# Performance work log

Measured on AMD Instinct MI355X. Metric: run time of the kernel, lower is better.

## Reference

```python
import jax, jax.numpy as jnp
import numpy as np

N = 207      # node_size (METR-LA)
E = 1722     # edge_size from edge CSV
RES = 12     # resolution
T = 288 // RES  # time-of-day slots


def setup_inputs() -> dict:
    key = jax.random.key(0)
    ks = jax.random.split(key, 12)
    B, L = 64, 2048
    return {
        "inputs": jax.random.normal(ks[0], (B, 2, N, L), jnp.float32),
        "ind": jax.random.randint(ks[1], (B,), 0, 288),
        "edge_from": jax.random.randint(ks[2], (E,), 0, N),
        "edge_to": jax.random.randint(ks[3], (E,), 0, N),
        "weight_react": jax.random.normal(ks[4], (T, E), jnp.float32) / 10.0,
        "weight_diff": jax.random.normal(ks[5], (T, E), jnp.float32) / 1000.0,
        "weight_react_a": jax.random.normal(ks[6], (T, E), jnp.float32) / 10.0,
        "weight_diff_a": jax.random.normal(ks[7], (T, E), jnp.float32) / 1000.0,
        "bias_reaction": jax.random.normal(ks[8], (T, N), jnp.float32) / 10.0,
        "bias_diffusion": jax.random.normal(ks[9], (T, N), jnp.float32) / 10.0,
        "bias_reaction_a": jax.random.normal(ks[10], (T, N), jnp.float32) / 10.0,
        "bias_diffusion_a": jax.random.normal(ks[11], (T, N), jnp.float32) / 10.0,
    }


def _scatter(w, src, dst):
    # dense NxN from edge list; duplicate edges accumulate (torch sparse coalesce semantics)
    return jnp.zeros((N, N), w.dtype).at[src, dst].add(w)


def _diag_colsum(A):
    # torch.sum(A, 1) on [1,N,N] sums over the first node axis -> column sums
    return jax.vmap(jnp.diag)(A.sum(axis=1))


def reference(inputs, ind, edge_from, edge_to,
              weight_react, weight_diff, weight_react_a, weight_diff_a,
              bias_reaction, bias_diffusion, bias_reaction_a, bias_diffusion_a):
    x = inputs[:, 0, :, :]              # [B, N, L]
    ii = ind // RES                      # [B] time-slot indices

    scat = jax.vmap(_scatter, in_axes=(0, None, None))
    Ar = scat(weight_react[ii], edge_from, edge_to)      # [B,N,N] index = (i, j)
    Ad = scat(weight_diff[ii], edge_to, edge_from)       # index_a = (j, i)
    Ara = scat(weight_react_a[ii], edge_from, edge_to)
    Ada = scat(weight_diff_a[ii], edge_to, edge_from)

    RW = _diag_colsum(Ar) - Ar           # Laplacian: D - A
    DW = _diag_colsum(Ad) - Ad
    RWa = _diag_colsum(Ara) + Ara        # D + A
    # faithful replication: batch element 0 uses diag of colsums of the already-built
    # reaction Laplacian (I1 - A) instead of reaction_weight_a (original-code quirk)
    RWa = RWa.at[0].set(jnp.diag(RW[0].sum(axis=0)) + Ara[0])
    DWa = _diag_colsum(Ada) + Ada

    conv = lambda A: jnp.einsum('nvl,nwv->nwl', x, A)   # out[n,w,l] = sum_v A[n,w,v] x[n,v,l]
    reaction = conv(RW) + bias_reaction[ii][:, :, None]
    reaction_a = conv(RWa) + bias_reaction_a[ii][:, :, None]
    diffusion = conv(DW) + bias_diffusion[ii][:, :, None]
    diffusion_a = conv(DWa) + bias_diffusion_a[ii][:, :, None]

    return jnp.tanh(reaction) + jnp.tanh(reaction_a) + diffusion + diffusion_a + x
```

## Files before the change

kernel.cpp:

```cpp
#include <hip/hip_runtime.h>
#include <cstdint>
#include <cstddef>

#define NN 207
#define NE 1722
#define NT 24
#define LL 2048
#define LCC 256
#define EPMAX 2560


typedef float f2 __attribute__((ext_vector_type(2)));

__device__ __forceinline__ f2 tanh2(f2 x) {
    f2 o;
    float ex = __expf(2.0f * x.x), ey = __expf(2.0f * x.y);
    o.x = 1.0f - __fdividef(2.0f, ex + 1.0f);
    o.y = 1.0f - __fdividef(2.0f, ey + 1.0f);
    return o;
}

__device__ __forceinline__ f2 up2(unsigned int u) {
    f2 v;
    v.x = __uint_as_float(u << 16);
    v.y = __uint_as_float(u & 0xffff0000u);
    return v;
}

__device__ __forceinline__ unsigned short bf16_rne(float f) {
    unsigned int u = __float_as_uint(f);
    u += 0x7FFFu + ((u >> 16) & 1u);
    return (unsigned short)(u >> 16);
}

__device__ __forceinline__ f2 fma2(float s, f2 x, f2 a) {
    f2 sv = s;
    return __builtin_elementwise_fma(sv, x, a);
}

__global__ void k_build_csr(const int* __restrict__ efrom, const int* __restrict__ eto,
                            int* __restrict__ rp_f, int* __restrict__ rp_t,
                            int* __restrict__ perm_f, unsigned short* __restrict__ nbr16_f,
                            int* __restrict__ perm_t, unsigned short* __restrict__ nbr16_t) {
    __shared__ int cf[NN], ctn[NN], curf[NN], curt[NN];
    const int tid = threadIdx.x;
    for (int w = tid; w < NN; w += 256) { cf[w] = 0; ctn[w] = 0; }
    __syncthreads();
    for (int e = tid; e < NE; e += 256) {
        atomicAdd(&cf[efrom[e]], 1);
        atomicAdd(&ctn[eto[e]], 1);
    }
    __syncthreads();
    if (tid == 0) {
        int p = 0;
        for (int w = 0; w < NN; w++) { rp_f[w] = p; curf[w] = p; p += (cf[w] + 3) & ~3; }
        rp_f[NN] = p;
    }
    if (tid == 64) {
        int p = 0;
        for (int w = 0; w < NN; w++) { rp_t[w] = p; curt[w] = p; p += (ctn[w] + 3) & ~3; }
        rp_t[NN] = p;
    }
    __syncthreads();
    for (int j = tid; j < EPMAX; j += 256) {
        perm_f[j] = -1; perm_t[j] = -1; nbr16_f[j] = 0; nbr16_t[j] = 0;
    }
    __syncthreads();
    for (int e = tid; e < NE; e += 256) {
        int w  = efrom[e];
        int p  = atomicAdd(&curf[w], 1);
        perm_f[p] = e; nbr16_f[p] = (unsigned short)eto[e];
        int w2 = eto[e];
        int p2 = atomicAdd(&curt[w2], 1);
        perm_t[p2] = e; nbr16_t[p2] = (unsigned short)efrom[e];
    }
}

__global__ void k_build_records(const int* __restrict__ perm_f, const int* __restrict__ perm_t,
                                const float* __restrict__ wr, const float* __restrict__ wra,
                                const float* __restrict__ wd, const float* __restrict__ wda,
                                f2* __restrict__ wf_f, f2* __restrict__ wf_t) {
    int gid = blockIdx.x * 256 + threadIdx.x;
    int t = gid / EPMAX;
    int j = gid - t * EPMAX;
    if (t >= NT) return;
    int ef = perm_f[j];
    f2 a; a.x = 0.0f; a.y = 0.0f;
    if (ef >= 0) { a.x = wr[t * NE + ef]; a.y = wra[t * NE + ef]; }
    wf_f[gid] = a;
    int et = perm_t[j];
    f2 b; b.x = 0.0f; b.y = 0.0f;
    if (et >= 0) { b.x = wd[t * NE + et]; b.y = wda[t * NE + et]; }
    wf_t[gid] = b;
}

__global__ void k_build_tables(const int* __restrict__ rp_f, const int* __restrict__ rp_t,
                               const int* __restrict__ perm_f, const int* __restrict__ perm_t,
                               const float* __restrict__ wr, const float* __restrict__ wra,
                               const float* __restrict__ wd, const float* __restrict__ wda,
                               const float* __restrict__ br, const float* __restrict__ bd,
                               const float* __restrict__ bra, const float* __restrict__ bda,
                               float4* __restrict__ ct4, float4* __restrict__ bb4) {
    int gid = blockIdx.x * 256 + threadIdx.x;
    if (gid >= NT * NN) return;
    int t = gid / NN;
    int w = gid - t * NN;
    float cr = 0.0f, cra = 0.0f, cd = 0.0f, cda = 0.0f;
    for (int j = rp_t[w]; j < rp_t[w + 1]; j++) {
        int eid = perm_t[j];
        if (eid >= 0) { cr += wr[t * NE + eid]; cra += wra[t * NE + eid]; }
    }
    for (int j = rp_f[w]; j < rp_f[w + 1]; j++) {
        int eid = perm_f[j];
        if (eid >= 0) { cd += wd[t * NE + eid]; cda += wda[t * NE + eid]; }
    }
    ct4[gid] = make_float4(cr, cra, cd, cda);
    bb4[gid] = make_float4(br[gid], bra[gid], bd[gid], bda[gid]);
}

__global__ __launch_bounds__(512, 2) void k_main(
    const float* __restrict__ inputs, const int* __restrict__ ind,
    const int* __restrict__ rp_f, const int* __restrict__ rp_t,
    const unsigned short* __restrict__ nbr16_f, const unsigned short* __restrict__ nbr16_t,
    const f2* __restrict__ wf_f, const f2* __restrict__ wf_t,
    const float4* __restrict__ ct4, const float4* __restrict__ bb4,
    float* __restrict__ out) {
    __shared__ f2 lw_f[EPMAX];
    __shared__ f2 lw_t[EPMAX];
    __shared__ unsigned short xs[NN * LCC];
    __shared__ unsigned short lnbr_f[EPMAX];
    __shared__ unsigned short lnbr_t[EPMAX];
    __shared__ int lrp_f[NN + 1];
    __shared__ int lrp_t[NN + 1];

    const int b     = blockIdx.y;
    const int chunk = blockIdx.x;
    const int tid   = threadIdx.x;
    const int t     = ind[b] / 12;

    {
        const f2* wff = wf_f + (size_t)t * EPMAX;
        const f2* wft = wf_t + (size_t)t * EPMAX;
        for (int i = tid; i < EPMAX; i += 512) {
            lw_f[i] = wff[i];
            lw_t[i] = wft[i];
            lnbr_f[i] = nbr16_f[i];
            lnbr_t[i] = nbr16_t[i];
        }
        for (int i = tid; i <= NN; i += 512) { lrp_f[i] = rp_f[i]; lrp_t[i] = rp_t[i]; }
    }
    const float* xbase = inputs + ((size_t)b * 2 * NN) * LL + (size_t)chunk * LCC;
    for (int i = tid; i < NN * 64; i += 512) {
        int row = i >> 6;
        int c4  = (i & 63) << 2;
        float4 v = *(const float4*)(xbase + (size_t)row * LL + c4);
        ushort4 h;
        h.x = bf16_rne(v.x);
        h.y = bf16_rne(v.y);
        h.z = bf16_rne(v.z);
        h.w = bf16_rne(v.w);
        *(ushort4*)&xs[row * LCC + c4] = h;
    }
    __syncthreads();

    const int l  = tid & 63;
    const int w0 = tid >> 6;
    const unsigned int lbase = (unsigned int)l * 8u;
    const char* xsb = (const char*)xs;
    const float4* ct4p = ct4 + (size_t)t * NN;
    const float4* bb4p = bb4 + (size_t)t * NN;
    float* outb = out + ((size_t)b * NN) * LL + (size_t)chunk * LCC + 4 * l;

    int w = w0;
    int f0 = lrp_f[w], f1 = lrp_f[w + 1], g0 = lrp_t[w], g1 = lrp_t[w + 1];
    float4 cc = ct4p[w], bbv = bb4p[w];

    for (int k = 0; k < 26; k++, w += 8) {
        if (w >= NN) break;
        int wn = w + 8;
        int nf0 = 0, nf1 = 0, ng0 = 0, ng1 = 0;
        float4 ncc = make_float4(0, 0, 0, 0), nbb = make_float4(0, 0, 0, 0);
        if (wn < NN) {
            nf0 = lrp_f[wn]; nf1 = lrp_f[wn + 1]; ng0 = lrp_t[wn]; ng1 = lrp_t[wn + 1];
            ncc = ct4p[wn]; nbb = bb4p[wn];
        }

        uint2 gxw = *(const uint2*)(xsb + (unsigned int)w * (LCC * 2) + lbase);
        f2 xlo = up2(gxw.x), xhi = up2(gxw.y);
        float cra = (b == 0) ? 0.0f : cc.y;
        f2 r_lo  = fma2(cc.x, xlo, (f2)bbv.x), r_hi  = fma2(cc.x, xhi, (f2)bbv.x);
        f2 ra_lo = fma2(cra,  xlo, (f2)bbv.y), ra_hi = fma2(cra,  xhi, (f2)bbv.y);
        f2 d_lo  = fma2(cc.z, xlo, (f2)bbv.z), d_hi  = fma2(cc.z, xhi, (f2)bbv.z);
        f2 da_lo = fma2(cc.w, xlo, (f2)bbv.w), da_hi = fma2(cc.w, xhi, (f2)bbv.w);

        for (int j = f0; j < f1; j += 4) {
            #pragma unroll
            for (int u = 0; u < 4; u++) {
                unsigned int n = lnbr_f[j + u];
                f2 wv = lw_f[j + u];
                uint2 g = *(const uint2*)(xsb + n * (LCC * 2) + lbase);
                f2 x_lo = up2(g.x), x_hi = up2(g.y);
                r_lo  = fma2(-wv.x, x_lo, r_lo);  r_hi  = fma2(-wv.x, x_hi, r_hi);
                ra_lo = fma2( wv.y, x_lo, ra_lo); ra_hi = fma2( wv.y, x_hi, ra_hi);
            }
        }
        for (int j = g0; j < g1; j += 4) {
            #pragma unroll
            for (int u = 0; u < 4; u++) {
                unsigned int n = lnbr_t[j + u];
                f2 wv = lw_t[j + u];
                uint2 g = *(const uint2*)(xsb + n * (LCC * 2) + lbase);
                f2 x_lo = up2(g.x), x_hi = up2(g.y);
                d_lo  = fma2(-wv.x, x_lo, d_lo);  d_hi  = fma2(-wv.x, x_hi, d_hi);
                da_lo = fma2( wv.y, x_lo, da_lo); da_hi = fma2( wv.y, x_hi, da_hi);
            }
        }

        f2 o_lo = tanh2(r_lo) + tanh2(ra_lo) + d_lo + da_lo + xlo;
        f2 o_hi = tanh2(r_hi) + tanh2(ra_hi) + d_hi + da_hi + xhi;
        float4 ov; ov.x = o_lo.x; ov.y = o_lo.y; ov.z = o_hi.x; ov.w = o_hi.y;
        *(float4*)(outb + (size_t)w * LL) = ov;

        f0 = nf0; f1 = nf1; g0 = ng0; g1 = ng1; cc = ncc; bbv = nbb;
    }
}

extern "C" void kernel_launch(void* const* d_in, const int* in_sizes, int n_in,
                              void* d_out, int out_size, void* d_ws, size_t ws_size,
                              hipStream_t stream) {
    const float* inputs = (const float*)d_in[0];
    const int*   ind    = (const int*)d_in[1];
    const int*   efrom  = (const int*)d_in[2];
    const int*   eto    = (const int*)d_in[3];
    const float* wr     = (const float*)d_in[4];
    const float* wd     = (const float*)d_in[5];
    const float* wra    = (const float*)d_in[6];
    const float* wda    = (const float*)d_in[7];
    const float* br     = (const float*)d_in[8];
    const float* bd     = (const float*)d_in[9];
    const float* bra    = (const float*)d_in[10];
    const float* bda    = (const float*)d_in[11];
    float* out = (float*)d_out;

    char* ws = (char*)d_ws;
    int*            rp_f    = (int*)(ws + 0);
    int*            rp_t    = (int*)(ws + 1024);
    int*            perm_f  = (int*)(ws + 2048);
    int*            perm_t  = (int*)(ws + 12288);
    unsigned short* nbr16_f = (unsigned short*)(ws + 22528);
    unsigned short* nbr16_t = (unsigned short*)(ws + 27648);
    f2*             wf_f    = (f2*)(ws + 32768);
    f2*             wf_t    = (f2*)(ws + 524288);
    float4*         ct4     = (float4*)(ws + 1015808);
    float4*         bb4     = (float4*)(ws + 1095296);

    const int B = in_sizes[1];

    k_build_csr<<<dim3(1), dim3(256), 0, stream>>>(efrom, eto, rp_f, rp_t,
                                                   perm_f, nbr16_f, perm_t, nbr16_t);
    k_build_records<<<dim3(NT * EPMAX / 256), dim3(256), 0, stream>>>(
        perm_f, perm_t, wr, wra, wd, wda, wf_f, wf_t);
    k_build_tables<<<dim3((NT * NN + 255) / 256), dim3(256), 0, stream>>>(
        rp_f, rp_t, perm_f, perm_t, wr, wra, wd, wda, br, bd, bra, bda, ct4, bb4);
    k_main<<<dim3(LL / LCC, B), dim3(512), 0, stream>>>(
        inputs, ind, rp_f, rp_t, nbr16_f, nbr16_t, wf_f, wf_t, ct4, bb4, out);
}
```

Measured before the change: 442.7 us.

## Replace CSR sparse gather with dense fp16 MFMA GEMM over prebuilt adjacency tiles

Drops the CSR-based sparse neighbor gather. Each time slot's adjacency is now densified into fp16 16x16x32 MFMA A-fragments, with the two diffusion matrices merged into one. The main kernel transposes an fp16 x tile into LDS and runs dense matrix-core GEMMs, adding diagonal and bias terms in the epilogue. This trades the irregular LDS gathers and scalar FMAs for far more nominal FLOPs on matrix cores, and switches the input precision from bf16 to fp16.

```diff
diff --git a/kernel.cpp b/kernel.cpp
--- a/kernel.cpp
+++ b/kernel.cpp
@@ -6,222 +6,176 @@
 #define NE 1722
 #define NT 24
 #define LL 2048
-#define LCC 256
-#define EPMAX 2560
-
-
-typedef float f2 __attribute__((ext_vector_type(2)));
-
-__device__ __forceinline__ f2 tanh2(f2 x) {
-    f2 o;
-    float ex = __expf(2.0f * x.x), ey = __expf(2.0f * x.y);
-    o.x = 1.0f - __fdividef(2.0f, ex + 1.0f);
-    o.y = 1.0f - __fdividef(2.0f, ey + 1.0f);
-    return o;
-}
-
-__device__ __forceinline__ f2 up2(unsigned int u) {
-    f2 v;
-    v.x = __uint_as_float(u << 16);
-    v.y = __uint_as_float(u & 0xffff0000u);
-    return v;
-}
-
-__device__ __forceinline__ unsigned short bf16_rne(float f) {
-    unsigned int u = __float_as_uint(f);
-    u += 0x7FFFu + ((u >> 16) & 1u);
-    return (unsigned short)(u >> 16);
-}
-
-__device__ __forceinline__ f2 fma2(float s, f2 x, f2 a) {
-    f2 sv = s;
-    return __builtin_elementwise_fma(sv, x, a);
-}
-
-__global__ void k_build_csr(const int* __restrict__ efrom, const int* __restrict__ eto,
-                            int* __restrict__ rp_f, int* __restrict__ rp_t,
-                            int* __restrict__ perm_f, unsigned short* __restrict__ nbr16_f,
-                            int* __restrict__ perm_t, unsigned short* __restrict__ nbr16_t) {
-    __shared__ int cf[NN], ctn[NN], curf[NN], curt[NN];
+#define LCC 128
+#define KP  224
+#define KS  228
+#define MTILES 13
+#define KTILES 7
+
+
+typedef float   f32x4 __attribute__((ext_vector_type(4)));
+typedef _Float16 half8 __attribute__((ext_vector_type(8)));
+
+__device__ __forceinline__ unsigned short f2h(float f) {
+    return __builtin_bit_cast(unsigned short, (_Float16)f);
+}
+__device__ __forceinline__ float tanhfast(float z) {
+    return 1.0f - __fdividef(2.0f, __expf(2.0f * z) + 1.0f);
+}
+
+__global__ void k_build(const int* __restrict__ efrom, const int* __restrict__ eto,
+                        const float* __restrict__ wr, const float* __restrict__ wd,
+                        const float* __restrict__ wra, const float* __restrict__ wda,
+                        const float* __restrict__ br, const float* __restrict__ bd,
+                        const float* __restrict__ bra, const float* __restrict__ bda,
+                        unsigned short* __restrict__ Wpack,
+                        float4* __restrict__ cb4, float4* __restrict__ bb4) {
+    const int t   = blockIdx.x / MTILES;
+    const int mt  = blockIdx.x % MTILES;
     const int tid = threadIdx.x;
-    for (int w = tid; w < NN; w += 256) { cf[w] = 0; ctn[w] = 0; }
-    __syncthreads();
+    __shared__ float rowbuf[3][16][KP];
+    __shared__ float cs[4][16];
+
+    float* rb = &rowbuf[0][0][0];
+    for (int i = tid; i < 3 * 16 * KP; i += 256) rb[i] = 0.0f;
+    if (tid < 64) ((float*)cs)[tid] = 0.0f;
+    __syncthreads();
+
+    const int mt16 = mt * 16;
+    const float* wrt  = wr  + (size_t)t * NE;
+    const float* wdt  = wd  + (size_t)t * NE;
+    const float* wrat = wra + (size_t)t * NE;
+    const float* wdat = wda + (size_t)t * NE;
     for (int e = tid; e < NE; e += 256) {
-        atomicAdd(&cf[efrom[e]], 1);
-        atomicAdd(&ctn[eto[e]], 1);
-    }
-    __syncthreads();
-    if (tid == 0) {
-        int p = 0;
-        for (int w = 0; w < NN; w++) { rp_f[w] = p; curf[w] = p; p += (cf[w] + 3) & ~3; }
-        rp_f[NN] = p;
-    }
-    if (tid == 64) {
-        int p = 0;
-        for (int w = 0; w < NN; w++) { rp_t[w] = p; curt[w] = p; p += (ctn[w] + 3) & ~3; }
-        rp_t[NN] = p;
-    }
-    __syncthreads();
-    for (int j = tid; j < EPMAX; j += 256) {
-        perm_f[j] = -1; perm_t[j] = -1; nbr16_f[j] = 0; nbr16_t[j] = 0;
-    }
-    __syncthreads();
-    for (int e = tid; e < NE; e += 256) {
-        int w  = efrom[e];
-        int p  = atomicAdd(&curf[w], 1);
-        perm_f[p] = e; nbr16_f[p] = (unsigned short)eto[e];
-        int w2 = eto[e];
-        int p2 = atomicAdd(&curt[w2], 1);
-        perm_t[p2] = e; nbr16_t[p2] = (unsigned short)efrom[e];
-    }
-}
-
-__global__ void k_build_records(const int* __restrict__ perm_f, const int* __restrict__ perm_t,
-                                const float* __restrict__ wr, const float* __restrict__ wra,
-                                const float* __restrict__ wd, const float* __restrict__ wda,
-                                f2* __restrict__ wf_f, f2* __restrict__ wf_t) {
-    int gid = blockIdx.x * 256 + threadIdx.x;
-    int t = gid / EPMAX;
-    int j = gid - t * EPMAX;
-    if (t >= NT) return;
-    int ef = perm_f[j];
-    f2 a; a.x = 0.0f; a.y = 0.0f;
-    if (ef >= 0) { a.x = wr[t * NE + ef]; a.y = wra[t * NE + ef]; }
-    wf_f[gid] = a;
-    int et = perm_t[j];
-    f2 b; b.x = 0.0f; b.y = 0.0f;
-    if (et >= 0) { b.x = wd[t * NE + et]; b.y = wda[t * NE + et]; }
-    wf_t[gid] = b;
-}
-
-__global__ void k_build_tables(const int* __restrict__ rp_f, const int* __restrict__ rp_t,
-                               const int* __restrict__ perm_f, const int* __restrict__ perm_t,
-                               const float* __restrict__ wr, const float* __restrict__ wra,
-                               const float* __restrict__ wd, const float* __restrict__ wda,
-                               const float* __restrict__ br, const float* __restrict__ bd,
-                               const float* __restrict__ bra, const float* __restrict__ bda,
-                               float4* __restrict__ ct4, float4* __restrict__ bb4) {
-    int gid = blockIdx.x * 256 + threadIdx.x;
-    if (gid >= NT * NN) return;
-    int t = gid / NN;
-    int w = gid - t * NN;
-    float cr = 0.0f, cra = 0.0f, cd = 0.0f, cda = 0.0f;
-    for (int j = rp_t[w]; j < rp_t[w + 1]; j++) {
-        int eid = perm_t[j];
-        if (eid >= 0) { cr += wr[t * NE + eid]; cra += wra[t * NE + eid]; }
-    }
-    for (int j = rp_f[w]; j < rp_f[w + 1]; j++) {
-        int eid = perm_f[j];
-        if (eid >= 0) { cd += wd[t * NE + eid]; cda += wda[t * NE + eid]; }
-    }
-    ct4[gid] = make_float4(cr, cra, cd, cda);
-    bb4[gid] = make_float4(br[gid], bra[gid], bd[gid], bda[gid]);
-}
-
-__global__ __launch_bounds__(512, 2) void k_main(
+        int ef = efrom[e], et = eto[e];
+        unsigned rf = (unsigned)(ef - mt16), rt = (unsigned)(et - mt16);
+        bool in_f = rf < 16u, in_t = rt < 16u;
+        if (in_f || in_t) {
+            float w1 = wrt[e], w2 = wdt[e], w3 = wrat[e], w4 = wdat[e];
+            if (in_t) {
+                atomicAdd(&rowbuf[2][rt][ef], w4 - w2);
+                atomicAdd(&cs[0][rt], w1);
+                atomicAdd(&cs[1][rt], w3);
+            }
+            if (in_f) {
+                atomicAdd(&rowbuf[0][rf][et], -w1);
+                atomicAdd(&rowbuf[1][rf][et],  w3);
+                atomicAdd(&cs[2][rf], w2);
+                atomicAdd(&cs[3][rf], w4);
+            }
+        }
+    }
+    __syncthreads();
+
+    if (tid < 16) {
+        int w = mt16 + tid;
+        if (w < NN) {
+            cb4[t * NN + w] = make_float4(cs[0][tid], cs[1][tid], cs[2][tid] + cs[3][tid], 0.0f);
+            bb4[t * NN + w] = make_float4(br[t * NN + w], bra[t * NN + w],
+                                          bd[t * NN + w] + bda[t * NN + w], 0.0f);
+        }
+    }
+
+    for (int fr = tid; fr < 3 * KTILES * 64; fr += 256) {
+        int mat = fr / (KTILES * 64);
+        int rem = fr - mat * (KTILES * 64);
+        int ks = rem >> 6, l = rem & 63;
+        int r = l & 15, g = l >> 4;
+        const float* src = &rowbuf[mat][r][0];
+        unsigned short h[8];
+        #pragma unroll
+        for (int e2 = 0; e2 < 4; ++e2) h[e2]     = f2h(src[ks * 32 + 4 * g + e2]);
+        #pragma unroll
+        for (int e2 = 0; e2 < 4; ++e2) h[4 + e2] = f2h(src[ks * 32 + 16 + 4 * g + e2]);
+        uint4 pv;
+        pv.x = (unsigned)h[0] | ((unsigned)h[1] << 16);
+        pv.y = (unsigned)h[2] | ((unsigned)h[3] << 16);
+        pv.z = (unsigned)h[4] | ((unsigned)h[5] << 16);
+        pv.w = (unsigned)h[6] | ((unsigned)h[7] << 16);
+        size_t o = ((size_t)(((t * MTILES + mt) * 3 + mat) * KTILES + ks) * 64 + l) * 8;
+        *(uint4*)(Wpack + o) = pv;
+    }
+}
+
+__global__ __launch_bounds__(512, 4) void k_mfma(
     const float* __restrict__ inputs, const int* __restrict__ ind,
-    const int* __restrict__ rp_f, const int* __restrict__ rp_t,
-    const unsigned short* __restrict__ nbr16_f, const unsigned short* __restrict__ nbr16_t,
-    const f2* __restrict__ wf_f, const f2* __restrict__ wf_t,
-    const float4* __restrict__ ct4, const float4* __restrict__ bb4,
+    const unsigned short* __restrict__ Wpack,
+    const float4* __restrict__ cb4, const float4* __restrict__ bb4,
     float* __restrict__ out) {
-    __shared__ f2 lw_f[EPMAX];
-    __shared__ f2 lw_t[EPMAX];
-    __shared__ unsigned short xs[NN * LCC];
-    __shared__ unsigned short lnbr_f[EPMAX];
-    __shared__ unsigned short lnbr_t[EPMAX];
-    __shared__ int lrp_f[NN + 1];
-    __shared__ int lrp_t[NN + 1];
-
-    const int b     = blockIdx.y;
-    const int chunk = blockIdx.x;
-    const int tid   = threadIdx.x;
-    const int t     = ind[b] / 12;
-
+    __shared__ unsigned short xT[LCC * KS];
+    __shared__ float4 lcb[NN], lbb[NN];
+    const int b = blockIdx.y, chunk = blockIdx.x, tid = threadIdx.x;
+    const int t = ind[b] / 12;
+
+    for (int i = tid; i < NN; i += 512) { lcb[i] = cb4[t * NN + i]; lbb[i] = bb4[t * NN + i]; }
     {
-        const f2* wff = wf_f + (size_t)t * EPMAX;
-        const f2* wft = wf_t + (size_t)t * EPMAX;
-        for (int i = tid; i < EPMAX; i += 512) {
-            lw_f[i] = wff[i];
-            lw_t[i] = wft[i];
-            lnbr_f[i] = nbr16_f[i];
-            lnbr_t[i] = nbr16_t[i];
-        }
-        for (int i = tid; i <= NN; i += 512) { lrp_f[i] = rp_f[i]; lrp_t[i] = rp_t[i]; }
-    }
-    const float* xbase = inputs + ((size_t)b * 2 * NN) * LL + (size_t)chunk * LCC;
-    for (int i = tid; i < NN * 64; i += 512) {
-        int row = i >> 6;
-        int c4  = (i & 63) << 2;
-        float4 v = *(const float4*)(xbase + (size_t)row * LL + c4);
-        ushort4 h;
-        h.x = bf16_rne(v.x);
-        h.y = bf16_rne(v.y);
-        h.z = bf16_rne(v.z);
-        h.w = bf16_rne(v.w);
-        *(ushort4*)&xs[row * LCC + c4] = h;
-    }
-    __syncthreads();
-
-    const int l  = tid & 63;
-    const int w0 = tid >> 6;
-    const unsigned int lbase = (unsigned int)l * 8u;
-    const char* xsb = (const char*)xs;
-    const float4* ct4p = ct4 + (size_t)t * NN;
-    const float4* bb4p = bb4 + (size_t)t * NN;
-    float* outb = out + ((size_t)b * NN) * LL + (size_t)chunk * LCC + 4 * l;
-
-    int w = w0;
-    int f0 = lrp_f[w], f1 = lrp_f[w + 1], g0 = lrp_t[w], g1 = lrp_t[w + 1];
-    float4 cc = ct4p[w], bbv = bb4p[w];
-
-    for (int k = 0; k < 26; k++, w += 8) {
-        if (w >= NN) break;
-        int wn = w + 8;
-        int nf0 = 0, nf1 = 0, ng0 = 0, ng1 = 0;
-        float4 ncc = make_float4(0, 0, 0, 0), nbb = make_float4(0, 0, 0, 0);
-        if (wn < NN) {
-            nf0 = lrp_f[wn]; nf1 = lrp_f[wn + 1]; ng0 = lrp_t[wn]; ng1 = lrp_t[wn + 1];
-            ncc = ct4p[wn]; nbb = bb4p[wn];
-        }
-
-        uint2 gxw = *(const uint2*)(xsb + (unsigned int)w * (LCC * 2) + lbase);
-        f2 xlo = up2(gxw.x), xhi = up2(gxw.y);
-        float cra = (b == 0) ? 0.0f : cc.y;
-        f2 r_lo  = fma2(cc.x, xlo, (f2)bbv.x), r_hi  = fma2(cc.x, xhi, (f2)bbv.x);
-        f2 ra_lo = fma2(cra,  xlo, (f2)bbv.y), ra_hi = fma2(cra,  xhi, (f2)bbv.y);
-        f2 d_lo  = fma2(cc.z, xlo, (f2)bbv.z), d_hi  = fma2(cc.z, xhi, (f2)bbv.z);
-        f2 da_lo = fma2(cc.w, xlo, (f2)bbv.w), da_hi = fma2(cc.w, xhi, (f2)bbv.w);
-
-        for (int j = f0; j < f1; j += 4) {
-            #pragma unroll
-            for (int u = 0; u < 4; u++) {
-                unsigned int n = lnbr_f[j + u];
-                f2 wv = lw_f[j + u];
-                uint2 g = *(const uint2*)(xsb + n * (LCC * 2) + lbase);
-                f2 x_lo = up2(g.x), x_hi = up2(g.y);
-                r_lo  = fma2(-wv.x, x_lo, r_lo);  r_hi  = fma2(-wv.x, x_hi, r_hi);
-                ra_lo = fma2( wv.y, x_lo, ra_lo); ra_hi = fma2( wv.y, x_hi, ra_hi);
+        int4 z = make_int4(0, 0, 0, 0);
+        for (int i = tid; i < LCC * KS * 2 / 16; i += 512) ((int4*)xT)[i] = z;
+    }
+    __syncthreads();
+
+    const float* xb = inputs + (size_t)b * (2 * NN * LL) + (size_t)chunk * LCC;
+    for (int i = tid; i < NN * (LCC / 4); i += 512) {
+        int k = i >> 5;
+        int c4 = (i & 31) << 2;
+        float4 v = *(const float4*)(xb + (size_t)k * LL + c4);
+        xT[(c4 + 0) * KS + k] = f2h(v.x);
+        xT[(c4 + 1) * KS + k] = f2h(v.y);
+        xT[(c4 + 2) * KS + k] = f2h(v.z);
+        xT[(c4 + 3) * KS + k] = f2h(v.w);
+    }
+    __syncthreads();
+
+    const int l  = tid & 63, wv = tid >> 6;
+    const int r  = l & 15,  g  = l >> 4;
+    const int col = wv * 16 + r;
+
+    half8 bf[KTILES];
+    #pragma unroll
+    for (int ks = 0; ks < KTILES; ++ks) {
+        uint2 lo = *(const uint2*)&xT[col * KS + ks * 32 + 4 * g];
+        uint2 hi = *(const uint2*)&xT[col * KS + ks * 32 + 16 + 4 * g];
+        uint4 u; u.x = lo.x; u.y = lo.y; u.z = hi.x; u.w = hi.y;
+        bf[ks] = __builtin_bit_cast(half8, u);
+    }
+
+    const unsigned short* Ap = Wpack + (size_t)t * (MTILES * 3 * KTILES * 512) + (size_t)l * 8;
+    const float* xrd = inputs + (size_t)b * (2 * NN * LL) + (size_t)chunk * LCC + col;
+    float* ob = out + (size_t)b * ((size_t)NN * LL) + (size_t)chunk * LCC + col;
+
+    for (int mt = 0; mt < MTILES; ++mt) {
+        f32x4 aR = {0.f, 0.f, 0.f, 0.f};
+        f32x4 aA = {0.f, 0.f, 0.f, 0.f};
+        f32x4 aD = {0.f, 0.f, 0.f, 0.f};
+        #pragma unroll
+        for (int ks = 0; ks < KTILES; ++ks) {
+            half8 a = __builtin_bit_cast(half8, *(const uint4*)Ap); Ap += 512;
+            aR = __builtin_amdgcn_mfma_f32_16x16x32_f16(a, bf[ks], aR, 0, 0, 0);
+        }
+        #pragma unroll
+        for (int ks = 0; ks < KTILES; ++ks) {
+            half8 a = __builtin_bit_cast(half8, *(const uint4*)Ap); Ap += 512;
+            aA = __builtin_amdgcn_mfma_f32_16x16x32_f16(a, bf[ks], aA, 0, 0, 0);
+        }
+        #pragma unroll
+        for (int ks = 0; ks < KTILES; ++ks) {
+            half8 a = __builtin_bit_cast(half8, *(const uint4*)Ap); Ap += 512;
+            aD = __builtin_amdgcn_mfma_f32_16x16x32_f16(a, bf[ks], aD, 0, 0, 0);
+        }
+        const int rowb = mt * 16 + 4 * g;
+        #pragma unroll
+        for (int q = 0; q < 4; ++q) {
+            int row = rowb + q;
+            if (row < NN) {
+                float xq = xrd[(size_t)row * LL];
+                float4 cb = lcb[row], bb = lbb[row];
+                float rr = aR[q] + cb.x * xq + bb.x;
+                float ra = aA[q] + bb.y;
+                if (b != 0) ra += cb.y * xq;
+                float dd = aD[q] + cb.z * xq + bb.z;
+                ob[(size_t)row * LL] = tanhfast(rr) + tanhfast(ra) + dd + xq;
             }
         }
-        for (int j = g0; j < g1; j += 4) {
-            #pragma unroll
-            for (int u = 0; u < 4; u++) {
-                unsigned int n = lnbr_t[j + u];
-                f2 wv = lw_t[j + u];
-                uint2 g = *(const uint2*)(xsb + n * (LCC * 2) + lbase);
-                f2 x_lo = up2(g.x), x_hi = up2(g.y);
-                d_lo  = fma2(-wv.x, x_lo, d_lo);  d_hi  = fma2(-wv.x, x_hi, d_hi);
-                da_lo = fma2( wv.y, x_lo, da_lo); da_hi = fma2( wv.y, x_hi, da_hi);
-            }
-        }
-
-        f2 o_lo = tanh2(r_lo) + tanh2(ra_lo) + d_lo + da_lo + xlo;
-        f2 o_hi = tanh2(r_hi) + tanh2(ra_hi) + d_hi + da_hi + xhi;
-        float4 ov; ov.x = o_lo.x; ov.y = o_lo.y; ov.z = o_hi.x; ov.w = o_hi.y;
-        *(float4*)(outb + (size_t)w * LL) = ov;
-
-        f0 = nf0; f1 = nf1; g0 = ng0; g1 = ng1; cc = ncc; bbv = nbb;
     }
 }
 
@@ -243,25 +197,14 @@
     float* out = (float*)d_out;
 
     char* ws = (char*)d_ws;
-    int*            rp_f    = (int*)(ws + 0);
-    int*            rp_t    = (int*)(ws + 1024);
-    int*            perm_f  = (int*)(ws + 2048);
-    int*            perm_t  = (int*)(ws + 12288);
-    unsigned short* nbr16_f = (unsigned short*)(ws + 22528);
-    unsigned short* nbr16_t = (unsigned short*)(ws + 27648);
-    f2*             wf_f    = (f2*)(ws + 32768);
-    f2*             wf_t    = (f2*)(ws + 524288);
-    float4*         ct4     = (float4*)(ws + 1015808);
-    float4*         bb4     = (float4*)(ws + 1095296);
+    float4*         cb4   = (float4*)(ws + 0);
+    float4*         bb4   = (float4*)(ws + 79488);
+    unsigned short* Wpack = (unsigned short*)(ws + 158976);
 
     const int B = in_sizes[1];
 
-    k_build_csr<<<dim3(1), dim3(256), 0, stream>>>(efrom, eto, rp_f, rp_t,
-                                                   perm_f, nbr16_f, perm_t, nbr16_t);
-    k_build_records<<<dim3(NT * EPMAX / 256), dim3(256), 0, stream>>>(
-        perm_f, perm_t, wr, wra, wd, wda, wf_f, wf_t);
-    k_build_tables<<<dim3((NT * NN + 255) / 256), dim3(256), 0, stream>>>(
-        rp_f, rp_t, perm_f, perm_t, wr, wra, wd, wda, br, bd, bra, bda, ct4, bb4);
-    k_main<<<dim3(LL / LCC, B), dim3(512), 0, stream>>>(
-        inputs, ind, rp_f, rp_t, nbr16_f, nbr16_t, wf_f, wf_t, ct4, bb4, out);
-}
+    k_build<<<dim3(NT * MTILES), dim3(256), 0, stream>>>(
+        efrom, eto, wr, wd, wra, wda, br, bd, bra, bda, Wpack, cb4, bb4);
+    k_mfma<<<dim3(LL / LCC, B), dim3(512), 0, stream>>>(
+        inputs, ind, Wpack, cb4, bb4, out);
+}
```

Measured after the change: 418.7 us. -5.4%, faster.
